# Kernel optimization log

Hardware: AMD Instinct MI355X
Metric: run time of the kernel (lower is better)

## Reference

```python
import jax, jax.numpy as jnp
import numpy as np

B, Hn, Wn, C, NH, WS, SR = 4, 64, 64, 256, 8, 3, 8
HD = C // NH
N = Hn * Wn
L = WS * WS
PH, PW = Hn // SR, Wn // SR
P = PH * PW
T = 4096  # cpb table length
NEG = -1e30

def _l2norm(x, axis=-1):
    return x / jnp.maximum(jnp.linalg.norm(x, axis=axis, keepdims=True), 1e-12)

def _unfold(x, ws):
    # x: (B, C, H, W) -> (B, C, ws*ws, H*W), torch F.unfold channel ordering (C major)
    p = ws // 2
    b, c, h, w = x.shape
    xp = jnp.pad(x, ((0, 0), (0, 0), (p, p), (p, p)))
    pats = jnp.stack([xp[:, :, i:i + h, j:j + w] for i in range(ws) for j in range(ws)], axis=2)
    return pats.reshape(b, c, ws * ws, h * w)

def setup_inputs():
    key = jax.random.key(0)
    ks = jax.random.split(key, 16)
    def w(k, shape, s=0.02):
        return jax.random.normal(k, shape, jnp.float32) * s
    # buffers derived from the window geometry (get_seqlen_and_mask)
    ones = np.ones((Hn, Wn), np.float32)
    pad = WS // 2
    op = np.pad(ones, pad)
    pats = np.stack([op[i:i + Hn, j:j + Wn] for i in range(WS) for j in range(WS)], -1).reshape(N, L)
    padding_mask = jnp.asarray(pats == 0)
    seq_length_scale = jnp.asarray(np.log(pats.sum(-1, keepdims=True) + P).astype(np.float32))
    temperature = jnp.log(jnp.expm1(jnp.ones((NH, 1, 1), jnp.float32) / 0.24))
    return dict(
        x=jax.random.normal(ks[0], (B, N, C), jnp.float32),
        relative_pos_index=jax.random.randint(ks[1], (N, P), 0, T),
        relative_coords_table=jax.random.uniform(ks[2], (T, 2), jnp.float32, -1.0, 1.0),
        q_w=w(ks[3], (C, C)), q_b=jnp.zeros((C,), jnp.float32),
        kv_w=w(ks[4], (2 * C, C)), kv_b=jnp.zeros((2 * C,), jnp.float32),
        temperature=temperature,
        query_embedding=w(ks[5], (NH, 1, HD)),
        proj_w=w(ks[6], (C, C)), proj_b=jnp.zeros((C,), jnp.float32),
        sr_w=w(ks[7], (C, C)), sr_b=jnp.zeros((C,), jnp.float32),
        norm_g=jnp.ones((C,), jnp.float32), norm_b=jnp.zeros((C,), jnp.float32),
        cpb1_w=w(ks[8], (512, 2)), cpb1_b=jnp.zeros((512,), jnp.float32),
        cpb2_w=w(ks[9], (NH, 512)), cpb2_b=jnp.zeros((NH,), jnp.float32),
        rpb_local=w(ks[10], (NH, L), 0.0004),
        learnable_tokens=w(ks[11], (NH, HD, L)),
        learnable_bias=jnp.zeros((NH, 1, L), jnp.float32),
        seq_length_scale=seq_length_scale,
        padding_mask=padding_mask,
        H=Hn, W=Wn,
    )

def _forward(x, q_w, q_b, kv_w, kv_b, temperature, query_embedding, proj_w, proj_b,
             sr_w, sr_b, norm_g, norm_b, cpb1_w, cpb1_b, cpb2_w, cpb2_b, rpb_local,
             learnable_tokens, learnable_bias, seq_length_scale, relative_coords_table,
             relative_pos_index, padding_mask, H, W):
    b, n, c = x.shape
    # normalized queries, scaled by learnable temperature and log-seqlen
    q = (x @ q_w.T + q_b).reshape(b, n, NH, HD).transpose(0, 2, 1, 3)  # (B,h,N,d)
    q_norm = _l2norm(q)
    q_scaled = (q_norm + query_embedding[None]) * jax.nn.softplus(temperature)[None] * seq_length_scale
    # --- local branch: sliding-window QK with RPB ---
    kv = x @ kv_w.T + kv_b  # (B,N,2C)
    k_loc = _l2norm((kv[..., :c]).reshape(b, n, NH, HD)).reshape(b, n, c)
    kv_img = jnp.concatenate([k_loc, kv[..., c:]], -1).transpose(0, 2, 1).reshape(b, 2 * c, H, W)
    pats = _unfold(kv_img, WS).reshape(b, 2 * NH, HD, L, n).transpose(0, 1, 4, 2, 3)  # (B,2h,N,d,L)
    k_loc, v_loc = pats[:, :NH], pats[:, NH:]
    attn_local = jnp.einsum('bhnd,bhndl->bhnl', q_scaled, k_loc) + rpb_local[None, :, None, :]
    attn_local = jnp.where(padding_mask[None, None], NEG, attn_local)
    # --- pooled branch ---
    x_img = x.transpose(0, 2, 1).reshape(b, c, H, W)
    x_sr = jax.nn.gelu(jnp.einsum('bchw,oc->bohw', x_img, sr_w) + sr_b[None, :, None, None], approximate=False)
    x_pool = x_sr.reshape(b, c, PH, SR, PW, SR).mean((3, 5)).reshape(b, c, P).transpose(0, 2, 1)  # (B,P,C)
    mu = x_pool.mean(-1, keepdims=True)
    var = x_pool.var(-1, keepdims=True)
    x_pool = (x_pool - mu) / jnp.sqrt(var + 1e-5) * norm_g + norm_b
    kv_pool = (x_pool @ kv_w.T + kv_b).reshape(b, P, 2 * NH, HD).transpose(0, 2, 1, 3)
    k_pool, v_pool = kv_pool[:, :NH], kv_pool[:, NH:]  # (B,h,P,d)
    cpb = jax.nn.relu(relative_coords_table @ cpb1_w.T + cpb1_b) @ cpb2_w.T + cpb2_b  # (T,h)
    pool_bias = cpb.T[:, relative_pos_index.reshape(-1)].reshape(NH, n, P)
    attn_pool = jnp.einsum('bhnd,bhpd->bhnp', q_scaled, _l2norm(k_pool)) + pool_bias[None]
    # --- joint softmax over local + pooled keys ---
    attn = jax.nn.softmax(jnp.concatenate([attn_local, attn_pool], -1), axis=-1)
    attn_local, attn_pool = attn[..., :L], attn[..., L:]
    a = jnp.einsum('bhnd,hdl->bhnl', q_norm, learnable_tokens) + learnable_bias[None] + attn_local
    x_local = jnp.einsum('bhnl,bhndl->bhnd', a, v_loc)
    x_pool_out = jnp.einsum('bhnp,bhpd->bhnd', attn_pool, v_pool)
    out = (x_local + x_pool_out).transpose(0, 2, 1, 3).reshape(b, n, c)
    return out @ proj_w.T + proj_b

def reference(x, relative_pos_index, relative_coords_table, q_w, q_b, kv_w, kv_b, temperature,
              query_embedding, proj_w, proj_b, sr_w, sr_b, norm_g, norm_b, cpb1_w, cpb1_b,
              cpb2_w, cpb2_b, rpb_local, learnable_tokens, learnable_bias, seq_length_scale,
              padding_mask, H, W):
    return _forward(x, q_w, q_b, kv_w, kv_b, temperature, query_embedding, proj_w, proj_b,
                    sr_w, sr_b, norm_g, norm_b, cpb1_w, cpb1_b, cpb2_w, cpb2_b, rpb_local,
                    learnable_tokens, learnable_bias, seq_length_scale, relative_coords_table,
                    relative_pos_index, padding_mask, H, W)
```

## Files before the change

kernel.cpp:

```cpp
#include <hip/hip_runtime.h>
#include <hip/hip_bf16.h>

typedef unsigned short u16;
typedef unsigned int u32;

#define B_ 4
#define N_ 4096
#define C_ 256
#define NH_ 8
#define HD_ 32
#define L_ 9
#define P_ 64
#define T_ 4096
#define NEG_ (-1e30f)

typedef __attribute__((ext_vector_type(8))) short bf16x8;
typedef __attribute__((ext_vector_type(4))) float f32x4;

__device__ __forceinline__ float b2f(u16 u) {
    union { u32 i; float f; } v; v.i = ((u32)u) << 16; return v.f;
}
__device__ __forceinline__ u16 f2b(float f) {
    u32 x = __float_as_uint(f);
    u32 r = (x + 0x7fffu + ((x >> 16) & 1u)) >> 16;
    return (u16)r;
}
__device__ __forceinline__ short f2bs(float f) { return (short)f2b(f); }

__global__ __launch_bounds__(256) void prep_k(
    const float* __restrict__ x, const float* __restrict__ q_w, const float* __restrict__ kv_w,
    const float* __restrict__ sr_w, const float* __restrict__ proj_w,
    u16* __restrict__ xb, u16* __restrict__ wfused, u16* __restrict__ pwb,
    const float* __restrict__ table, const float* __restrict__ w1, const float* __restrict__ b1,
    const float* __restrict__ w2, const float* __restrict__ b2, float* __restrict__ cpb)
{
    __shared__ float w1s[512][2];
    __shared__ float b1s[512];
    __shared__ float w2s[8][512];
    int bid = blockIdx.x, tid = threadIdx.x;
    if (bid < 4096) {
        int i = bid * 256 + tid;
        float4 v = reinterpret_cast<const float4*>(x)[i];
        ushort4 o; o.x = f2b(v.x); o.y = f2b(v.y); o.z = f2b(v.z); o.w = f2b(v.w);
        reinterpret_cast<ushort4*>(xb)[i] = o;
    } else if (bid < 4416) {
        int i = (bid - 4096) * 256 + tid;
        const float* s; u16* d; int off;
        if (i < 16384)      { s = q_w;    d = wfused; off = i; }
        else if (i < 49152) { s = kv_w;   d = wfused; off = i; }
        else if (i < 65536) { s = sr_w;   d = wfused; off = i; }
        else                { s = proj_w; d = pwb;    off = i - 65536; }
        int soff = (i < 16384) ? i : (i < 49152) ? (i - 16384) : (i < 65536) ? (i - 49152) : (i - 65536);
        float4 v = reinterpret_cast<const float4*>(s)[soff];
        ushort4 o; o.x = f2b(v.x); o.y = f2b(v.y); o.z = f2b(v.z); o.w = f2b(v.w);
        reinterpret_cast<ushort4*>(d)[off] = o;
    } else {
        for (int i = tid; i < 512; i += 256) {
            w1s[i][0] = w1[i * 2]; w1s[i][1] = w1[i * 2 + 1]; b1s[i] = b1[i];
        }
        for (int i = tid; i < 4096; i += 256) w2s[i >> 9][i & 511] = w2[i];
        __syncthreads();
        int t = (bid - 4416) * 256 + tid;
        float t0 = table[t * 2], t1 = table[t * 2 + 1];
        float acc[8] = {};
        for (int j = 0; j < 512; ++j) {
            float h = fmaxf(t0 * w1s[j][0] + t1 * w1s[j][1] + b1s[j], 0.0f);
            #pragma unroll
            for (int hh = 0; hh < 8; ++hh) acc[hh] += h * w2s[hh][j];
        }
        #pragma unroll
        for (int hh = 0; hh < 8; ++hh) cpb[t * 8 + hh] = acc[hh] + b2[hh];
    }
}

template<int MODE>
__global__ __launch_bounds__(256) void gemm_big_k(
    const u16* __restrict__ A, const u16* __restrict__ W,
    const float* __restrict__ b0, const float* __restrict__ b1, const float* __restrict__ b2,
    float* __restrict__ qn, float* __restrict__ kv, u16* __restrict__ xgb, float* __restrict__ pout)
{
    constexpr int RI = (MODE == 0) ? 4 : 1;
    __shared__ u16 Bs[64 * 264];
    int tid = threadIdx.x, w = tid >> 6, lane = tid & 63;
    int quad = lane >> 4, l16 = lane & 15;
    int colBase = blockIdx.x * 64;
    #pragma unroll
    for (int c = 0; c < 8; ++c) {
        int linear = c * 256 + tid;
        int col = linear >> 5, kc = linear & 31;
        uint4 v = *reinterpret_cast<const uint4*>(W + (size_t)(colBase + col) * 256 + kc * 8);
        *reinterpret_cast<uint4*>(&Bs[col * 264 + kc * 8]) = v;
    }
    __syncthreads();
    int rowBase = blockIdx.y * (RI * 64) + w * (RI * 16);
    f32x4 acc[RI][4] = {};
    const u16* aptr = A + (size_t)(rowBase + l16) * 256 + quad * 8;
    bf16x8 afc[RI];
    #pragma unroll
    for (int i = 0; i < RI; ++i) afc[i] = *reinterpret_cast<const bf16x8*>(aptr + (size_t)i * 16 * 256);
    #pragma unroll
    for (int k0 = 0; k0 < 256; k0 += 32) {
        bf16x8 afn[RI];
        if (k0 < 224) {
            #pragma unroll
            for (int i = 0; i < RI; ++i)
                afn[i] = *reinterpret_cast<const bf16x8*>(aptr + (size_t)i * 16 * 256 + k0 + 32);
        }
        #pragma unroll
        for (int j = 0; j < 4; ++j) {
            bf16x8 bfr = *reinterpret_cast<const bf16x8*>(&Bs[(j * 16 + l16) * 264 + k0 + quad * 8]);
            #pragma unroll
            for (int i = 0; i < RI; ++i)
                acc[i][j] = __builtin_amdgcn_mfma_f32_16x16x32_bf16(afc[i], bfr, acc[i][j], 0, 0, 0);
        }
        if (k0 < 224) {
            #pragma unroll
            for (int i = 0; i < RI; ++i) afc[i] = afn[i];
        }
    }
    int rng = (MODE == 0) ? (colBase >> 8) : 99;
    float bj[4];
    #pragma unroll
    for (int j = 0; j < 4; ++j) {
        int gc = colBase + j * 16 + l16;
        if (MODE == 1)      bj[j] = b0[gc];
        else if (rng == 0)  bj[j] = b0[gc];
        else if (rng <= 2)  bj[j] = b1[gc - 256];
        else                bj[j] = b2[gc - 768];
    }
    #pragma unroll
    for (int i = 0; i < RI; ++i) {
        float vals[4][4];
        #pragma unroll
        for (int j = 0; j < 4; ++j)
            #pragma unroll
            for (int r = 0; r < 4; ++r) {
                float t = acc[i][j][r] + bj[j];
                if (MODE == 0 && rng == 3) t = 0.5f * t * (1.0f + erff(t * 0.70710678118654752f));
                vals[j][r] = t;
            }
        if (MODE == 0 && rng <= 1) {
            #pragma unroll
            for (int hp = 0; hp < 2; ++hp)
                #pragma unroll
                for (int r = 0; r < 4; ++r) {
                    float s = vals[2*hp][r] * vals[2*hp][r] + vals[2*hp+1][r] * vals[2*hp+1][r];
                    s += __shfl_xor(s, 1); s += __shfl_xor(s, 2);
                    s += __shfl_xor(s, 4); s += __shfl_xor(s, 8);
                    float inv = 1.0f / fmaxf(sqrtf(s), 1e-12f);
                    vals[2*hp][r] *= inv; vals[2*hp+1][r] *= inv;
                }
        }
        #pragma unroll
        for (int j = 0; j < 4; ++j) {
            int gc = colBase + j * 16 + l16;
            #pragma unroll
            for (int r = 0; r < 4; ++r) {
                int row = rowBase + i * 16 + quad * 4 + r;
                if (MODE == 1)      pout[(size_t)row * 256 + gc] = vals[j][r];
                else if (rng == 0)  qn[(size_t)row * 256 + gc] = vals[j][r];
                else if (rng <= 2)  kv[(size_t)row * 512 + gc - 256] = vals[j][r];
                else                xgb[(size_t)row * 256 + gc - 768] = f2b(vals[j][r]);
            }
        }
    }
}

__global__ __launch_bounds__(256) void poolkv_k(
    const u16* __restrict__ xgb, const float* __restrict__ g, const float* __restrict__ bta,
    const float* __restrict__ kv_w, const float* __restrict__ kv_b, float* __restrict__ kvp)
{
    __shared__ __align__(16) float xps[256];
    __shared__ float r1[4], r2[4];
    int bid = blockIdx.x;
    int bp = bid >> 1, half = bid & 1;
    int b = bp >> 6, p = bp & 63;
    int py = p >> 3, px = p & 7;
    int o = threadIdx.x;
    float s = 0.0f;
    for (int sy = 0; sy < 8; ++sy)
        #pragma unroll
        for (int sx = 0; sx < 8; ++sx) {
            int pix = (py * 8 + sy) * 64 + px * 8 + sx;
            s += b2f(xgb[((size_t)(b * N_ + pix)) * C_ + o]);
        }
    float v = s * (1.0f / 64.0f);
    float s1 = v, s2 = v * v;
    #pragma unroll
    for (int off = 32; off >= 1; off >>= 1) { s1 += __shfl_xor(s1, off); s2 += __shfl_xor(s2, off); }
    int wv = o >> 6, ln = o & 63;
    if (ln == 0) { r1[wv] = s1; r2[wv] = s2; }
    __syncthreads();
    float S1 = r1[0] + r1[1] + r1[2] + r1[3];
    float S2 = r2[0] + r2[1] + r2[2] + r2[3];
    float mu = S1 * (1.0f / 256.0f);
    float var = S2 * (1.0f / 256.0f) - mu * mu;
    xps[o] = (v - mu) * rsqrtf(var + 1e-5f) * g[o] + bta[o];
    __syncthreads();
    int col = half * 256 + o;
    float a = kv_b[col];
    const float4* xp4 = (const float4*)xps;
    const float4* wrow = (const float4*)(kv_w + (size_t)col * 256);
    #pragma unroll 8
    for (int k4 = 0; k4 < 64; ++k4) {
        float4 xv = xp4[k4]; float4 wa = wrow[k4];
        a += xv.x * wa.x + xv.y * wa.y + xv.z * wa.z + xv.w * wa.w;
    }
    if (half == 0) {
        float ss = a * a;
        ss += __shfl_xor(ss, 1); ss += __shfl_xor(ss, 2); ss += __shfl_xor(ss, 4);
        ss += __shfl_xor(ss, 8); ss += __shfl_xor(ss, 16);
        a *= 1.0f / fmaxf(sqrtf(ss), 1e-12f);
    }
    kvp[(size_t)bp * 512 + col] = a;
}

__global__ __launch_bounds__(256) void attn_k(
    const float* __restrict__ qn, const float* __restrict__ kv,
    const float* __restrict__ kvp, const float* __restrict__ cpb,
    const int* __restrict__ rpi, const float* __restrict__ temp,
    const float* __restrict__ qe, const float* __restrict__ lt,
    const float* __restrict__ rpb, const float* __restrict__ lb,
    const float* __restrict__ slsin, u16* __restrict__ aob)
{
    __shared__ u16 kp_hi[64 * 40], kp_lo[64 * 40];
    __shared__ u16 vp_hi[32 * 72], vp_lo[32 * 72];
    __shared__ u16 ltb[16 * 32];
    __shared__ float S_w[4][16][76];
    __shared__ float rpb_s[9], lb_s[9];

    int bid = blockIdx.x;
    int tile = bid & 63, h = (bid >> 6) & 7, b = bid >> 9;
    int tid = threadIdx.x, wave = tid >> 6, lane = tid & 63;
    int quad = lane >> 4, l16 = lane & 15;

    {
        int p = tid >> 2, dc = (tid & 3) * 8;
        const float* src = kvp + ((size_t)(b * P_ + p)) * 512 + h * 32 + dc;
        float4 k0 = *(const float4*)(src), k1 = *(const float4*)(src + 4);
        float4 v0 = *(const float4*)(src + 256), v1 = *(const float4*)(src + 260);
        float kf[8] = {k0.x,k0.y,k0.z,k0.w,k1.x,k1.y,k1.z,k1.w};
        float vf[8] = {v0.x,v0.y,v0.z,v0.w,v1.x,v1.y,v1.z,v1.w};
        #pragma unroll
        for (int j = 0; j < 8; ++j) {
            u16 khi = f2b(kf[j]);
            kp_hi[p * 40 + dc + j] = khi;
            kp_lo[p * 40 + dc + j] = f2b(kf[j] - b2f(khi));
            u16 vhi = f2b(vf[j]);
            vp_hi[(dc + j) * 72 + p] = vhi;
            vp_lo[(dc + j) * 72 + p] = f2b(vf[j] - b2f(vhi));
        }
    }
    for (int t = tid; t < 512; t += 256) {
        int l = t & 15, d = t >> 4;
        ltb[l * 32 + d] = (l < 9) ? f2b(lt[h * 288 + d * 9 + l]) : (u16)0;
    }
    if (tid < 9) { rpb_s[tid] = rpb[h * 9 + tid]; lb_s[tid] = lb[h * 9 + tid]; }
    float tsc = log1pf(expf(temp[h]));
    __syncthreads();

    int n0w = tile * 64 + wave * 16;
    bf16x8 qs_hi, qs_lo, qn_b;
    float qsr[8];
    {
        int n = n0w + l16;
        const float* qptr = qn + ((size_t)(b * N_ + n)) * C_ + h * 32 + quad * 8;
        float4 q0 = *(const float4*)qptr, q1 = *(const float4*)(qptr + 4);
        const float* qeptr = qe + h * 32 + quad * 8;
        float4 e0 = *(const float4*)qeptr, e1 = *(const float4*)(qeptr + 4);
        float slv = slsin[n];
        float qf[8] = {q0.x,q0.y,q0.z,q0.w,q1.x,q1.y,q1.z,q1.w};
        float ef[8] = {e0.x,e0.y,e0.z,e0.w,e1.x,e1.y,e1.z,e1.w};
        #pragma unroll
        for (int j = 0; j < 8; ++j) {
            float qs = (qf[j] + ef[j]) * tsc * slv;
            u16 hi = f2b(qs);
            qs_hi[j] = (short)hi;
            qs_lo[j] = f2bs(qs - b2f(hi));
            qn_b[j]  = f2bs(qf[j]);
            qsr[j] = qs;
        }
        if (quad == 0) { S_w[wave][l16][73] = NEG_; S_w[wave][l16][74] = NEG_; S_w[wave][l16][75] = NEG_; }
    }

    #pragma unroll
    for (int jt = 0; jt < 4; ++jt) {
        bf16x8 bh = *(const bf16x8*)&kp_hi[(jt * 16 + l16) * 40 + quad * 8];
        bf16x8 bl = *(const bf16x8*)&kp_lo[(jt * 16 + l16) * 40 + quad * 8];
        f32x4 a = {};
        a = __builtin_amdgcn_mfma_f32_16x16x32_bf16(qs_lo, bh, a, 0, 0, 0);
        a = __builtin_amdgcn_mfma_f32_16x16x32_bf16(qs_hi, bl, a, 0, 0, 0);
        a = __builtin_amdgcn_mfma_f32_16x16x32_bf16(qs_hi, bh, a, 0, 0, 0);
        #pragma unroll
        for (int r = 0; r < 4; ++r) {
            int pix = quad * 4 + r;
            int n = n0w + pix;
            int idx = rpi[n * P_ + jt * 16 + l16];
            S_w[wave][pix][jt * 16 + l16] = a[r] + cpb[(size_t)idx * 8 + h];
        }
    }
    f32x4 accL;
    {
        bf16x8 ltf = *(const bf16x8*)&ltb[l16 * 32 + quad * 8];
        f32x4 z = {};
        accL = __builtin_amdgcn_mfma_f32_16x16x32_bf16(qn_b, ltf, z, 0, 0, 0);
    }
    #pragma unroll
    for (int l = 0; l < 9; ++l) {
        int n = n0w + l16, y = n >> 6, x = n & 63;
        int ny = y + l / 3 - 1, nx = x + (l % 3) - 1;
        bool ok = ((unsigned)ny < 64u) && ((unsigned)nx < 64u);
        int nn = ok ? ny * 64 + nx : n;
        const float4* kb = (const float4*)(kv + ((size_t)(b * N_ + nn)) * 512 + h * 32 + quad * 8);
        float4 k0v = kb[0], k1v = kb[1];
        float part = qsr[0]*k0v.x + qsr[1]*k0v.y + qsr[2]*k0v.z + qsr[3]*k0v.w
                   + qsr[4]*k1v.x + qsr[5]*k1v.y + qsr[6]*k1v.z + qsr[7]*k1v.w;
        part += __shfl_xor(part, 16);
        part += __shfl_xor(part, 32);
        if (quad == 0) S_w[wave][l16][64 + l] = ok ? (part + rpb_s[l]) : NEG_;
    }
    {
        int pix = lane >> 2, c0 = (lane & 3) * 19;
        float vals[19]; float mx = NEG_;
        #pragma unroll
        for (int i = 0; i < 19; ++i) { vals[i] = S_w[wave][pix][c0 + i]; mx = fmaxf(mx, vals[i]); }
        mx = fmaxf(mx, __shfl_xor(mx, 1));
        mx = fmaxf(mx, __shfl_xor(mx, 2));
        float sm = 0.0f;
        #pragma unroll
        for (int i = 0; i < 19; ++i) { vals[i] = expf(vals[i] - mx); sm += vals[i]; }
        sm += __shfl_xor(sm, 1); sm += __shfl_xor(sm, 2);
        float inv = 1.0f / sm;
        #pragma unroll
        for (int i = 0; i < 19; ++i) S_w[wave][pix][c0 + i] = vals[i] * inv;
    }
    if (l16 < 9) {
        #pragma unroll
        for (int r = 0; r < 4; ++r) {
            int pix = quad * 4 + r;
            int n = n0w + pix, y = n >> 6, x = n & 63;
            int ny = y + l16 / 3 - 1, nx = x + (l16 % 3) - 1;
            bool ok = ((unsigned)ny < 64u) && ((unsigned)nx < 64u);
            float prev = S_w[wave][pix][64 + l16];
            S_w[wave][pix][64 + l16] = ok ? (accL[r] + lb_s[l16] + prev) : 0.0f;
        }
    }
    f32x4 accO[2] = {};
    #pragma unroll
    for (int kc = 0; kc < 2; ++kc) {
        float wf[8];
        *(float4*)&wf[0] = *(const float4*)&S_w[wave][l16][kc * 32 + quad * 8];
        *(float4*)&wf[4] = *(const float4*)&S_w[wave][l16][kc * 32 + quad * 8 + 4];
        bf16x8 w_hi, w_lo;
        #pragma unroll
        for (int j = 0; j < 8; ++j) {
            u16 hi = f2b(wf[j]);
            w_hi[j] = (short)hi;
            w_lo[j] = f2bs(wf[j] - b2f(hi));
        }
        #pragma unroll
        for (int nt = 0; nt < 2; ++nt) {
            bf16x8 vh = *(const bf16x8*)&vp_hi[(nt * 16 + l16) * 72 + kc * 32 + quad * 8];
            bf16x8 vl = *(const bf16x8*)&vp_lo[(nt * 16 + l16) * 72 + kc * 32 + quad * 8];
            accO[nt] = __builtin_amdgcn_mfma_f32_16x16x32_bf16(w_lo, vh, accO[nt], 0, 0, 0);
            accO[nt] = __builtin_amdgcn_mfma_f32_16x16x32_bf16(w_hi, vl, accO[nt], 0, 0, 0);
            accO[nt] = __builtin_amdgcn_mfma_f32_16x16x32_bf16(w_hi, vh, accO[nt], 0, 0, 0);
        }
    }
    #pragma unroll
    for (int r = 0; r < 4; ++r) {
        int pix = quad * 4 + r;
        int n = n0w + pix, y = n >> 6, x = n & 63;
        #pragma unroll
        for (int l = 0; l < 9; ++l) {
            int ny = y + l / 3 - 1, nx = x + (l % 3) - 1;
            bool ok = ((unsigned)ny < 64u) && ((unsigned)nx < 64u);
            int nn = ok ? ny * 64 + nx : n;
            float aw = S_w[wave][pix][64 + l];
            const float* vb = kv + ((size_t)(b * N_ + nn)) * 512 + 256 + h * 32;
            accO[0][r] += aw * vb[l16];
            accO[1][r] += aw * vb[16 + l16];
        }
    }
    #pragma unroll
    for (int nt = 0; nt < 2; ++nt)
        #pragma unroll
        for (int r = 0; r < 4; ++r) {
            int n = n0w + quad * 4 + r;
            aob[((size_t)(b * N_ + n)) * C_ + h * 32 + nt * 16 + l16] = f2b(accO[nt][r]);
        }
}

extern "C" void kernel_launch(void* const* d_in, const int* in_sizes, int n_in,
                              void* d_out, int out_size, void* d_ws, size_t ws_size,
                              hipStream_t stream) {
    const float* x      = (const float*)d_in[0];
    const int*   rpi    = (const int*)d_in[1];
    const float* table  = (const float*)d_in[2];
    const float* q_w    = (const float*)d_in[3];
    const float* q_b    = (const float*)d_in[4];
    const float* kv_w   = (const float*)d_in[5];
    const float* kv_b   = (const float*)d_in[6];
    const float* temp   = (const float*)d_in[7];
    const float* qe     = (const float*)d_in[8];
    const float* proj_w = (const float*)d_in[9];
    const float* proj_b = (const float*)d_in[10];
    const float* sr_w   = (const float*)d_in[11];
    const float* sr_b   = (const float*)d_in[12];
    const float* norm_g = (const float*)d_in[13];
    const float* norm_b = (const float*)d_in[14];
    const float* cpb1_w = (const float*)d_in[15];
    const float* cpb1_b = (const float*)d_in[16];
    const float* cpb2_w = (const float*)d_in[17];
    const float* cpb2_b = (const float*)d_in[18];
    const float* rpb    = (const float*)d_in[19];
    const float* lt     = (const float*)d_in[20];
    const float* lb     = (const float*)d_in[21];
    const float* sls    = (const float*)d_in[22];

    float* ws  = (float*)d_ws;
    float* qn  = ws;
    float* kv  = qn  + (size_t)B_ * N_ * C_;
    float* kvp = kv  + (size_t)B_ * N_ * 2 * C_;
    float* cpb = kvp + (size_t)B_ * P_ * 2 * C_;
    u16*   xb  = (u16*)(cpb + (size_t)T_ * NH_);
    u16*   wfb = xb  + (size_t)B_ * N_ * C_;
    u16*   pwb = wfb + (size_t)1024 * C_;
    u16*   xgb = pwb + (size_t)C_ * C_;
    u16*   aob = xgb;

    dim3 blk(256);

    prep_k<<<dim3(4432), blk, 0, stream>>>(x, q_w, kv_w, sr_w, proj_w, xb, wfb, pwb,
                                           table, cpb1_w, cpb1_b, cpb2_w, cpb2_b, cpb);
    gemm_big_k<0><<<dim3(16, 64), blk, 0, stream>>>(xb, wfb, q_b, kv_b, sr_b, qn, kv, xgb, nullptr);
    poolkv_k<<<dim3(B_ * P_ * 2), blk, 0, stream>>>(xgb, norm_g, norm_b, kv_w, kv_b, kvp);
    attn_k<<<dim3(B_ * NH_ * 64), blk, 0, stream>>>(qn, kv, kvp, cpb, rpi, temp, qe, lt, rpb, lb, sls, aob);
    gemm_big_k<1><<<dim3(4, 256), blk, 0, stream>>>(aob, pwb, proj_b, nullptr, nullptr,
                                                    nullptr, nullptr, nullptr, (float*)d_out);
}
```

Measured before the change: 274.5 us.

## Fuse Q projection into attention, store V as bf16, pregather CPB bias

The Q projection and its L2 normalisation move out of the big GEMM and into the attention kernel, which computes them per tile with MFMA from the bf16 input and weights. This removes the fp32 qn round trip through memory. V is now stored as bf16, and K and V are split into separate contiguous buffers. The relative position bias is gathered once per head into a dense buffer in extra blocks of the pooling kernel, and the output projection GEMM processes two row tiles per wave. In exchange, Q is recomputed once per batch and head tile, V loses precision, and the bias buffer adds an 8 MB write and read.

```diff
diff --git a/kernel.cpp b/kernel.cpp
--- a/kernel.cpp
+++ b/kernel.cpp
@@ -77,13 +77,13 @@
 __global__ __launch_bounds__(256) void gemm_big_k(
     const u16* __restrict__ A, const u16* __restrict__ W,
     const float* __restrict__ b0, const float* __restrict__ b1, const float* __restrict__ b2,
-    float* __restrict__ qn, float* __restrict__ kv, u16* __restrict__ xgb, float* __restrict__ pout)
+    float* __restrict__ kvk, u16* __restrict__ kvv, u16* __restrict__ xgb, float* __restrict__ pout)
 {
-    constexpr int RI = (MODE == 0) ? 4 : 1;
+    constexpr int RI = (MODE == 0) ? 4 : 2;
     __shared__ u16 Bs[64 * 264];
     int tid = threadIdx.x, w = tid >> 6, lane = tid & 63;
     int quad = lane >> 4, l16 = lane & 15;
-    int colBase = blockIdx.x * 64;
+    int colBase = (MODE == 0 ? 256 : 0) + blockIdx.x * 64;
     #pragma unroll
     for (int c = 0; c < 8; ++c) {
         int linear = c * 256 + tid;
@@ -124,7 +124,6 @@
     for (int j = 0; j < 4; ++j) {
         int gc = colBase + j * 16 + l16;
         if (MODE == 1)      bj[j] = b0[gc];
-        else if (rng == 0)  bj[j] = b0[gc];
         else if (rng <= 2)  bj[j] = b1[gc - 256];
         else                bj[j] = b2[gc - 768];
     }
@@ -139,7 +138,7 @@
                 if (MODE == 0 && rng == 3) t = 0.5f * t * (1.0f + erff(t * 0.70710678118654752f));
                 vals[j][r] = t;
             }
-        if (MODE == 0 && rng <= 1) {
+        if (MODE == 0 && rng == 1) {
             #pragma unroll
             for (int hp = 0; hp < 2; ++hp)
                 #pragma unroll
@@ -158,8 +157,8 @@
             for (int r = 0; r < 4; ++r) {
                 int row = rowBase + i * 16 + quad * 4 + r;
                 if (MODE == 1)      pout[(size_t)row * 256 + gc] = vals[j][r];
-                else if (rng == 0)  qn[(size_t)row * 256 + gc] = vals[j][r];
-                else if (rng <= 2)  kv[(size_t)row * 512 + gc - 256] = vals[j][r];
+                else if (rng == 1)  kvk[(size_t)row * 256 + gc - 256] = vals[j][r];
+                else if (rng == 2)  kvv[(size_t)row * 256 + gc - 512] = f2b(vals[j][r]);
                 else                xgb[(size_t)row * 256 + gc - 768] = f2b(vals[j][r]);
             }
         }
@@ -168,15 +167,32 @@
 
 __global__ __launch_bounds__(256) void poolkv_k(
     const u16* __restrict__ xgb, const float* __restrict__ g, const float* __restrict__ bta,
-    const float* __restrict__ kv_w, const float* __restrict__ kv_b, float* __restrict__ kvp)
+    const float* __restrict__ kv_w, const float* __restrict__ kv_b, float* __restrict__ kvp,
+    const int* __restrict__ rpi, const float* __restrict__ cpb, float* __restrict__ biasp)
 {
+    int bid = blockIdx.x;
+    int tid = threadIdx.x;
+    if (bid >= 512) {
+        int i = (bid - 512) * 256 + tid;
+        int e0 = i * 4;
+        int p = e0 & 63;
+        int hn = e0 >> 6;
+        int n = hn & 4095, h = hn >> 12;
+        int4 idx4 = *reinterpret_cast<const int4*>(rpi + n * 64 + p);
+        float4 o;
+        o.x = cpb[(size_t)idx4.x * 8 + h];
+        o.y = cpb[(size_t)idx4.y * 8 + h];
+        o.z = cpb[(size_t)idx4.z * 8 + h];
+        o.w = cpb[(size_t)idx4.w * 8 + h];
+        *reinterpret_cast<float4*>(biasp + e0) = o;
+        return;
+    }
     __shared__ __align__(16) float xps[256];
     __shared__ float r1[4], r2[4];
-    int bid = blockIdx.x;
     int bp = bid >> 1, half = bid & 1;
     int b = bp >> 6, p = bp & 63;
     int py = p >> 3, px = p & 7;
-    int o = threadIdx.x;
+    int o = tid;
     float s = 0.0f;
     for (int sy = 0; sy < 8; ++sy)
         #pragma unroll
@@ -216,10 +232,10 @@
 }
 
 __global__ __launch_bounds__(256) void attn_k(
-    const float* __restrict__ qn, const float* __restrict__ kv,
-    const float* __restrict__ kvp, const float* __restrict__ cpb,
-    const int* __restrict__ rpi, const float* __restrict__ temp,
-    const float* __restrict__ qe, const float* __restrict__ lt,
+    const u16* __restrict__ xb, const u16* __restrict__ qwb, const float* __restrict__ q_b,
+    const float* __restrict__ kvk, const u16* __restrict__ kvv,
+    const float* __restrict__ kvp, const float* __restrict__ biasp,
+    const float* __restrict__ temp, const float* __restrict__ qe, const float* __restrict__ lt,
     const float* __restrict__ rpb, const float* __restrict__ lb,
     const float* __restrict__ slsin, u16* __restrict__ aob)
 {
@@ -227,6 +243,7 @@
     __shared__ u16 vp_hi[32 * 72], vp_lo[32 * 72];
     __shared__ u16 ltb[16 * 32];
     __shared__ float S_w[4][16][76];
+    __shared__ float qs_l[4][16][36];
     __shared__ float rpb_s[9], lb_s[9];
 
     int bid = blockIdx.x;
@@ -260,29 +277,56 @@
     __syncthreads();
 
     int n0w = tile * 64 + wave * 16;
+
+    f32x4 qacc[2] = {};
+    {
+        const u16* xrow = xb + ((size_t)(b * N_ + n0w + l16)) * 256 + quad * 8;
+        const u16* qwr  = qwb + ((size_t)(h * 32 + l16)) * 256 + quad * 8;
+        #pragma unroll
+        for (int k0 = 0; k0 < 256; k0 += 32) {
+            bf16x8 ax = *(const bf16x8*)(xrow + k0);
+            bf16x8 bw0 = *(const bf16x8*)(qwr + k0);
+            bf16x8 bw1 = *(const bf16x8*)(qwr + 16 * 256 + k0);
+            qacc[0] = __builtin_amdgcn_mfma_f32_16x16x32_bf16(ax, bw0, qacc[0], 0, 0, 0);
+            qacc[1] = __builtin_amdgcn_mfma_f32_16x16x32_bf16(ax, bw1, qacc[1], 0, 0, 0);
+        }
+    }
+    {
+        float qb0 = q_b[h * 32 + l16], qb1 = q_b[h * 32 + 16 + l16];
+        float qe0 = qe[h * 32 + l16],  qe1 = qe[h * 32 + 16 + l16];
+        #pragma unroll
+        for (int r = 0; r < 4; ++r) {
+            int p = quad * 4 + r;
+            float v0 = qacc[0][r] + qb0, v1 = qacc[1][r] + qb1;
+            float s = v0 * v0 + v1 * v1;
+            s += __shfl_xor(s, 1); s += __shfl_xor(s, 2);
+            s += __shfl_xor(s, 4); s += __shfl_xor(s, 8);
+            float inv = 1.0f / fmaxf(sqrtf(s), 1e-12f);
+            v0 *= inv; v1 *= inv;
+            float sc = tsc * slsin[n0w + p];
+            qs_l[wave][p][l16]      = (v0 + qe0) * sc;
+            qs_l[wave][p][16 + l16] = (v1 + qe1) * sc;
+        }
+        if (quad == 0) { S_w[wave][l16][73] = NEG_; S_w[wave][l16][74] = NEG_; S_w[wave][l16][75] = NEG_; }
+    }
     bf16x8 qs_hi, qs_lo, qn_b;
     float qsr[8];
     {
-        int n = n0w + l16;
-        const float* qptr = qn + ((size_t)(b * N_ + n)) * C_ + h * 32 + quad * 8;
-        float4 q0 = *(const float4*)qptr, q1 = *(const float4*)(qptr + 4);
-        const float* qeptr = qe + h * 32 + quad * 8;
-        float4 e0 = *(const float4*)qeptr, e1 = *(const float4*)(qeptr + 4);
-        float slv = slsin[n];
-        float qf[8] = {q0.x,q0.y,q0.z,q0.w,q1.x,q1.y,q1.z,q1.w};
+        *(float4*)&qsr[0] = *(const float4*)&qs_l[wave][l16][quad * 8];
+        *(float4*)&qsr[4] = *(const float4*)&qs_l[wave][l16][quad * 8 + 4];
+        float invs = 1.0f / (tsc * slsin[n0w + l16]);
+        const float* qep = qe + h * 32 + quad * 8;
+        float4 e0 = *(const float4*)qep, e1 = *(const float4*)(qep + 4);
         float ef[8] = {e0.x,e0.y,e0.z,e0.w,e1.x,e1.y,e1.z,e1.w};
         #pragma unroll
         for (int j = 0; j < 8; ++j) {
-            float qs = (qf[j] + ef[j]) * tsc * slv;
-            u16 hi = f2b(qs);
+            u16 hi = f2b(qsr[j]);
             qs_hi[j] = (short)hi;
-            qs_lo[j] = f2bs(qs - b2f(hi));
-            qn_b[j]  = f2bs(qf[j]);
-            qsr[j] = qs;
-        }
-        if (quad == 0) { S_w[wave][l16][73] = NEG_; S_w[wave][l16][74] = NEG_; S_w[wave][l16][75] = NEG_; }
-    }
-
+            qs_lo[j] = f2bs(qsr[j] - b2f(hi));
+            qn_b[j]  = f2bs(qsr[j] * invs - ef[j]);
+        }
+    }
+    const float* bp = biasp + (size_t)h * N_ * 64;
     #pragma unroll
     for (int jt = 0; jt < 4; ++jt) {
         bf16x8 bh = *(const bf16x8*)&kp_hi[(jt * 16 + l16) * 40 + quad * 8];
@@ -295,8 +339,7 @@
         for (int r = 0; r < 4; ++r) {
             int pix = quad * 4 + r;
             int n = n0w + pix;
-            int idx = rpi[n * P_ + jt * 16 + l16];
-            S_w[wave][pix][jt * 16 + l16] = a[r] + cpb[(size_t)idx * 8 + h];
+            S_w[wave][pix][jt * 16 + l16] = a[r] + bp[(size_t)n * 64 + jt * 16 + l16];
         }
     }
     f32x4 accL;
@@ -311,7 +354,7 @@
         int ny = y + l / 3 - 1, nx = x + (l % 3) - 1;
         bool ok = ((unsigned)ny < 64u) && ((unsigned)nx < 64u);
         int nn = ok ? ny * 64 + nx : n;
-        const float4* kb = (const float4*)(kv + ((size_t)(b * N_ + nn)) * 512 + h * 32 + quad * 8);
+        const float4* kb = (const float4*)(kvk + ((size_t)(b * N_ + nn)) * 256 + h * 32 + quad * 8);
         float4 k0v = kb[0], k1v = kb[1];
         float part = qsr[0]*k0v.x + qsr[1]*k0v.y + qsr[2]*k0v.z + qsr[3]*k0v.w
                    + qsr[4]*k1v.x + qsr[5]*k1v.y + qsr[6]*k1v.z + qsr[7]*k1v.w;
@@ -377,9 +420,9 @@
             bool ok = ((unsigned)ny < 64u) && ((unsigned)nx < 64u);
             int nn = ok ? ny * 64 + nx : n;
             float aw = S_w[wave][pix][64 + l];
-            const float* vb = kv + ((size_t)(b * N_ + nn)) * 512 + 256 + h * 32;
-            accO[0][r] += aw * vb[l16];
-            accO[1][r] += aw * vb[16 + l16];
+            const u16* vb = kvv + ((size_t)(b * N_ + nn)) * 256 + h * 32;
+            accO[0][r] += aw * b2f(vb[l16]);
+            accO[1][r] += aw * b2f(vb[16 + l16]);
         }
     }
     #pragma unroll
@@ -418,24 +461,26 @@
     const float* lb     = (const float*)d_in[21];
     const float* sls    = (const float*)d_in[22];
 
-    float* ws  = (float*)d_ws;
-    float* qn  = ws;
-    float* kv  = qn  + (size_t)B_ * N_ * C_;
-    float* kvp = kv  + (size_t)B_ * N_ * 2 * C_;
-    float* cpb = kvp + (size_t)B_ * P_ * 2 * C_;
-    u16*   xb  = (u16*)(cpb + (size_t)T_ * NH_);
-    u16*   wfb = xb  + (size_t)B_ * N_ * C_;
-    u16*   pwb = wfb + (size_t)1024 * C_;
-    u16*   xgb = pwb + (size_t)C_ * C_;
-    u16*   aob = xgb;
+    float* ws   = (float*)d_ws;
+    float* kvk  = ws;
+    float* kvp  = kvk + (size_t)B_ * N_ * C_;
+    float* cpb  = kvp + (size_t)B_ * P_ * 2 * C_;
+    float* bia  = cpb + (size_t)T_ * NH_;
+    u16*   xb   = (u16*)(bia + (size_t)NH_ * N_ * P_);
+    u16*   wfb  = xb  + (size_t)B_ * N_ * C_;
+    u16*   pwb  = wfb + (size_t)1024 * C_;
+    u16*   kvv  = pwb + (size_t)C_ * C_;
+    u16*   xgb  = kvv + (size_t)B_ * N_ * C_;
+    u16*   aob  = xgb;
 
     dim3 blk(256);
 
     prep_k<<<dim3(4432), blk, 0, stream>>>(x, q_w, kv_w, sr_w, proj_w, xb, wfb, pwb,
                                            table, cpb1_w, cpb1_b, cpb2_w, cpb2_b, cpb);
-    gemm_big_k<0><<<dim3(16, 64), blk, 0, stream>>>(xb, wfb, q_b, kv_b, sr_b, qn, kv, xgb, nullptr);
-    poolkv_k<<<dim3(B_ * P_ * 2), blk, 0, stream>>>(xgb, norm_g, norm_b, kv_w, kv_b, kvp);
-    attn_k<<<dim3(B_ * NH_ * 64), blk, 0, stream>>>(qn, kv, kvp, cpb, rpi, temp, qe, lt, rpb, lb, sls, aob);
-    gemm_big_k<1><<<dim3(4, 256), blk, 0, stream>>>(aob, pwb, proj_b, nullptr, nullptr,
+    gemm_big_k<0><<<dim3(12, 64), blk, 0, stream>>>(xb, wfb, nullptr, kv_b, sr_b, kvk, kvv, xgb, nullptr);
+    poolkv_k<<<dim3(2560), blk, 0, stream>>>(xgb, norm_g, norm_b, kv_w, kv_b, kvp, rpi, cpb, bia);
+    attn_k<<<dim3(B_ * NH_ * 64), blk, 0, stream>>>(xb, wfb, q_b, kvk, kvv, kvp, bia,
+                                                    temp, qe, lt, rpb, lb, sls, aob);
+    gemm_big_k<1><<<dim3(4, 128), blk, 0, stream>>>(aob, pwb, proj_b, nullptr, nullptr,
                                                     nullptr, nullptr, nullptr, (float*)d_out);
 }
```

New measurement: 266.3 us. 3.0% less time.
